# Kernel tuning notes

Hardware: AMD Instinct MI355X
Metric: run time of the kernel (lower is better)

## Reference

```python
import jax, jax.numpy as jnp
import numpy as np

B, T = 256, 20          # batch, sequence length
D = 128                 # encoder feature dim
H = 256                 # LSTM controller hidden / controller_output_size
KS = 256                # memory key/word size
MEM = 20                # memory slots
KNN = 4                 # k-NN addressing
Y = 4                   # output classes (y_dim)
EPS = 1e-8


def setup_inputs() -> dict:
    key = jax.random.key(0)
    ks = jax.random.split(key, 16)
    def kn(k, shape, fan_in):  # kaiming-normal-ish init
        return jax.random.normal(k, shape, jnp.float32) * np.float32(np.sqrt(2.0 / fan_in))
    return {
        "x": jax.random.normal(ks[0], (B, T, 32, 32), jnp.float32),
        # conv encoder
        "conv1_w": kn(ks[1], (32, 1, 4, 4), 1 * 16),  "conv1_b": jnp.zeros(32, jnp.float32),
        "conv2_w": kn(ks[2], (32, 32, 4, 4), 32 * 16), "conv2_b": jnp.zeros(32, jnp.float32),
        "conv3_w": kn(ks[3], (32, 32, 4, 4), 32 * 16), "conv3_b": jnp.zeros(32, jnp.float32),
        "fc1_w": kn(ks[4], (256, 512), 512), "fc1_b": jnp.zeros(256, jnp.float32),
        "fc2_w": kn(ks[5], (128, 256), 256), "fc2_b": jnp.zeros(128, jnp.float32),
        # context norm
        "gamma": jnp.ones(D, jnp.float32), "beta": jnp.zeros(D, jnp.float32),
        # LSTM controller: input = [z_t(128), read(256)] = 384
        "lstm_wi": kn(ks[6], (4 * H, D + KS), D + KS),
        "lstm_wh": kn(ks[7], (4 * H, H), H),
        "lstm_b": jnp.zeros(4 * H, jnp.float32),
        # head projections
        "wk": kn(ks[8], (KS, H), H),   # read key
        "wwk": kn(ks[9], (KS, H), H),  # write key
        "wv": kn(ks[10], (KS, H), H),  # write value
        # output layer on [h, read]
        "wo": kn(ks[11], (Y, H + KS), H + KS), "wo_b": jnp.zeros(Y, jnp.float32),
        "mem_init": jax.random.normal(ks[12], (MEM, KS), jnp.float32) * 0.01,
    }


def _conv(h, w, b):
    out = jax.lax.conv_general_dilated(h, w, (2, 2), [(1, 1), (1, 1)],
                                       dimension_numbers=("NCHW", "OIHW", "NCHW"))
    return jax.nn.relu(out + b[None, :, None, None])


def reference(x, conv1_w, conv1_b, conv2_w, conv2_b, conv3_w, conv3_b,
              fc1_w, fc1_b, fc2_w, fc2_b, gamma, beta,
              lstm_wi, lstm_wh, lstm_b, wk, wwk, wv, wo, wo_b, mem_init):
    b, t = x.shape[0], x.shape[1]
    # --- conv encoder on all B*T frames ---
    h = x.reshape(-1, 1, 32, 32)
    h = _conv(h, conv1_w, conv1_b)          # [BT,32,16,16]
    h = _conv(h, conv2_w, conv2_b)          # [BT,32,8,8]
    h = _conv(h, conv3_w, conv3_b)          # [BT,32,4,4]
    h = h.reshape(h.shape[0], -1)           # [BT,512] (NCHW flatten, matches torch)
    h = jax.nn.relu(h @ fc1_w.T + fc1_b)
    z = jax.nn.relu(h @ fc2_w.T + fc2_b).reshape(b, t, D)
    # --- context norm over time dim (torch var is unbiased) ---
    mu = z.mean(1)
    sigma = jnp.sqrt(z.var(1, ddof=1) + EPS)
    z = (z - mu[:, None, :]) / sigma[:, None, :] * gamma + beta
    # --- NTM-style MANN with k-NN addressing, scan over time ---
    zt = jnp.swapaxes(z, 0, 1)              # [T,B,D]
    M0 = jnp.broadcast_to(mem_init, (b, MEM, KS)) + jnp.zeros((b, MEM, KS), jnp.float32)
    carry0 = (jnp.zeros((b, H), jnp.float32), jnp.zeros((b, H), jnp.float32),
              jnp.zeros((b, KS), jnp.float32), M0)

    def step(carry, z_t):
        h_, c_, r_, M = carry
        inp = jnp.concatenate([z_t, r_], -1)
        gates = inp @ lstm_wi.T + h_ @ lstm_wh.T + lstm_b
        ig, fg, gg, og = jnp.split(gates, 4, -1)  # torch LSTM gate order i,f,g,o
        c_ = jax.nn.sigmoid(fg) * c_ + jax.nn.sigmoid(ig) * jnp.tanh(gg)
        h_ = jax.nn.sigmoid(og) * jnp.tanh(c_)
        Mn = M / (jnp.linalg.norm(M, axis=-1, keepdims=True) + EPS)
        def knn(kq):  # cosine sim -> top-k -> softmax weights
            kqn = kq / (jnp.linalg.norm(kq, axis=-1, keepdims=True) + EPS)
            sims = jnp.einsum('bd,bnd->bn', kqn, Mn)
            tv, ti = jax.lax.top_k(sims, KNN)
            return jax.nn.softmax(tv, -1), ti
        # read head
        wr, ir = knn(h_ @ wk.T)
        rows = jnp.take_along_axis(M, ir[..., None], axis=1)   # [B,KNN,KS] gather
        r_new = jnp.einsum('bk,bkd->bd', wr, rows)
        # write head: weighted scatter-add into top-k slots
        ws, iw = knn(h_ @ wwk.T)
        v = jnp.tanh(h_ @ wv.T)
        bidx = jnp.arange(M.shape[0])[:, None]
        M = M.at[bidx, iw].add(ws[..., None] * v[:, None, :])
        y = jnp.concatenate([h_, r_new], -1) @ wo.T + wo_b
        return (h_, c_, r_new, M), y

    _, ys = jax.lax.scan(step, carry0, zt)   # ys: [T,B,Y]
    y_pred_linear = ys[-1]
    return y_pred_linear, jnp.argmax(y_pred_linear, 1)
```

## Files before the change

### kernel.cpp

```cpp
#include <hip/hip_runtime.h>
#include <hip/hip_bf16.h>

#define EPSF 1e-8f

#define OFF_WIT 0
#define N_WIT   393216
#define OFF_WHT 393216
#define N_WHT   262144
#define OFF_PKT 655360
#define N_PKT   196608
#define OFF_F1T 851968
#define N_F1T   131072
#define OFF_F2T 983040
#define N_F2T   32768
#define OFF_Z   1015808
#define N_Z     655360
#define WS_FLOATS 1671168

__global__ __launch_bounds__(256) void pack_kernel(
    const float* __restrict__ wi, const float* __restrict__ wh,
    const float* __restrict__ wk, const float* __restrict__ wwk,
    const float* __restrict__ wv,
    const float* __restrict__ f1w, const float* __restrict__ f2w,
    float* __restrict__ ws) {
  int id = blockIdx.x * 256 + threadIdx.x;
  if (id < N_WIT) {
    int j = id & 3, r = (id >> 2) & 1023, k4 = id >> 12;
    ws[OFF_WIT + id] = wi[r * 384 + k4 * 4 + j];
    return;
  }
  id -= N_WIT;
  if (id < N_WHT) {
    int j = id & 3, r = (id >> 2) & 1023, k4 = id >> 12;
    ws[OFF_WHT + id] = wh[r * 256 + k4 * 4 + j];
    return;
  }
  id -= N_WHT;
  if (id < N_PKT) {
    int j = id & 3;
    int q = id >> 2;
    int c = q % 768, k4 = q / 768;
    int m = c >> 8, o = c & 255;
    int col = o * 256 + k4 * 4 + j;
    float v = (m == 0) ? wk[col] : (m == 1) ? wwk[col] : wv[col];
    ws[OFF_PKT + id] = v;
    return;
  }
  id -= N_PKT;
  if (id < N_F1T) {
    int m = id & 3, o = (id >> 2) & 255, k4 = id >> 10;
    ws[OFF_F1T + id] = f1w[o * 512 + k4 * 4 + m];
    return;
  }
  id -= N_F1T;
  if (id < N_F2T) {
    int m = id & 3, o = (id >> 2) & 127, k4 = id >> 9;
    ws[OFF_F2T + id] = f2w[o * 256 + k4 * 4 + m];
  }
}

__global__ __launch_bounds__(256) void enc_kernel(
    const float* __restrict__ x,
    const float* __restrict__ w1, const float* __restrict__ b1,
    const float* __restrict__ w2, const float* __restrict__ b2,
    const float* __restrict__ w3, const float* __restrict__ b3,
    const float* __restrict__ f1b, const float* __restrict__ f2b,
    float* __restrict__ ws) {
  __shared__ __align__(16) float xs[1024];
  __shared__ __align__(16) float c1s[512 * 19];
  __shared__ __align__(16) float c2s[256 * 9];
  __shared__ __align__(16) float c3s[512];
  __shared__ __align__(16) float h1s[256];

  const float4* __restrict__ f1T4 = (const float4*)(ws + OFF_F1T);
  const float4* __restrict__ f2T4 = (const float4*)(ws + OFF_F2T);
  float* __restrict__ z = ws + OFF_Z;

  const int f = blockIdx.x;
  const int tid = threadIdx.x;

  for (int i = tid; i < 1024; i += 256) xs[i] = x[f * 1024 + i];
  __syncthreads();

  {
    int oy = tid >> 4, ox = tid & 15;
    float patch[16];
    #pragma unroll
    for (int ky = 0; ky < 4; ++ky) {
      int iy = oy * 2 - 1 + ky;
      #pragma unroll
      for (int kx = 0; kx < 4; ++kx) {
        int ix = ox * 2 - 1 + kx;
        patch[ky * 4 + kx] =
            ((unsigned)iy <= 31u && (unsigned)ix <= 31u) ? xs[iy * 32 + ix] : 0.f;
      }
    }
    for (int oc = 0; oc < 32; ++oc) {
      float acc = b1[oc];
      #pragma unroll
      for (int k = 0; k < 16; ++k) acc = fmaf(patch[k], w1[oc * 16 + k], acc);
      c1s[(oc * 16 + oy) * 19 + ox] = fmaxf(acc, 0.f);
    }
  }
  __syncthreads();

  {
    int pix = tid & 63;
    int og = __builtin_amdgcn_readfirstlane(tid >> 6);
    int oy = pix >> 3, ox = pix & 7;
    float acc[8];
    #pragma unroll
    for (int j = 0; j < 8; ++j) acc[j] = b2[og * 8 + j];
    for (int ic = 0; ic < 32; ++ic) {
      float patch[16];
      #pragma unroll
      for (int ky = 0; ky < 4; ++ky) {
        int iy = oy * 2 - 1 + ky;
        #pragma unroll
        for (int kx = 0; kx < 4; ++kx) {
          int ix = ox * 2 - 1 + kx;
          patch[ky * 4 + kx] = ((unsigned)iy <= 15u && (unsigned)ix <= 15u)
                                   ? c1s[(ic * 16 + iy) * 19 + ix] : 0.f;
        }
      }
      #pragma unroll
      for (int j = 0; j < 8; ++j) {
        const float* wr = w2 + ((og * 8 + j) * 32 + ic) * 16;
        #pragma unroll
        for (int k = 0; k < 16; ++k) acc[j] = fmaf(patch[k], wr[k], acc[j]);
      }
    }
    #pragma unroll
    for (int j = 0; j < 8; ++j)
      c2s[((og * 8 + j) * 8 + oy) * 9 + ox] = fmaxf(acc[j], 0.f);
  }
  __syncthreads();

  {
    int pix = tid & 15, grp = tid >> 4;
    int oy = pix >> 2, ox = pix & 3;
    float a0 = b3[grp * 2], a1 = b3[grp * 2 + 1];
    for (int ic = 0; ic < 32; ++ic) {
      float patch[16];
      #pragma unroll
      for (int ky = 0; ky < 4; ++ky) {
        int iy = oy * 2 - 1 + ky;
        #pragma unroll
        for (int kx = 0; kx < 4; ++kx) {
          int ix = ox * 2 - 1 + kx;
          patch[ky * 4 + kx] = ((unsigned)iy <= 7u && (unsigned)ix <= 7u)
                                   ? c2s[(ic * 8 + iy) * 9 + ix] : 0.f;
        }
      }
      const float4* wa = (const float4*)(w3 + ((grp * 2 + 0) * 32 + ic) * 16);
      const float4* wb = (const float4*)(w3 + ((grp * 2 + 1) * 32 + ic) * 16);
      #pragma unroll
      for (int q = 0; q < 4; ++q) {
        float4 qa = wa[q], qb = wb[q];
        a0 = fmaf(patch[q * 4 + 0], qa.x, a0);
        a0 = fmaf(patch[q * 4 + 1], qa.y, a0);
        a0 = fmaf(patch[q * 4 + 2], qa.z, a0);
        a0 = fmaf(patch[q * 4 + 3], qa.w, a0);
        a1 = fmaf(patch[q * 4 + 0], qb.x, a1);
        a1 = fmaf(patch[q * 4 + 1], qb.y, a1);
        a1 = fmaf(patch[q * 4 + 2], qb.z, a1);
        a1 = fmaf(patch[q * 4 + 3], qb.w, a1);
      }
    }
    c3s[(grp * 2 + 0) * 16 + pix] = fmaxf(a0, 0.f);
    c3s[(grp * 2 + 1) * 16 + pix] = fmaxf(a1, 0.f);
  }
  __syncthreads();

  {
    float acc = f1b[tid];
    #pragma unroll 4
    for (int k4 = 0; k4 < 128; ++k4) {
      float4 cv = ((const float4*)c3s)[k4];
      float4 w = f1T4[k4 * 256 + tid];
      acc = fmaf(w.x, cv.x, acc);
      acc = fmaf(w.y, cv.y, acc);
      acc = fmaf(w.z, cv.z, acc);
      acc = fmaf(w.w, cv.w, acc);
    }
    h1s[tid] = fmaxf(acc, 0.f);
  }
  __syncthreads();

  if (tid < 128) {
    float acc = f2b[tid];
    #pragma unroll 4
    for (int k4 = 0; k4 < 64; ++k4) {
      float4 hv = ((const float4*)h1s)[k4];
      float4 w = f2T4[k4 * 128 + tid];
      acc = fmaf(w.x, hv.x, acc);
      acc = fmaf(w.y, hv.y, acc);
      acc = fmaf(w.z, hv.z, acc);
      acc = fmaf(w.w, hv.w, acc);
    }
    z[f * 128 + tid] = fmaxf(acc, 0.f);
  }
}

__global__ __launch_bounds__(256) void norm_kernel(
    float* __restrict__ ws,
    const float* __restrict__ gamma, const float* __restrict__ beta) {
  float* z = ws + OFF_Z;
  int g = blockIdx.x * 256 + threadIdx.x;
  int b = g >> 7, d = g & 127;
  float vals[20];
  float mu = 0.f;
  #pragma unroll
  for (int t = 0; t < 20; ++t) {
    float v = z[(b * 20 + t) * 128 + d];
    vals[t] = v;
    mu += v;
  }
  mu *= (1.f / 20.f);
  float var = 0.f;
  #pragma unroll
  for (int t = 0; t < 20; ++t) {
    float dd = vals[t] - mu;
    var = fmaf(dd, dd, var);
  }
  var *= (1.f / 19.f);
  float inv = 1.f / sqrtf(var + EPSF);
  float ga = gamma[d], be = beta[d];
  #pragma unroll
  for (int t = 0; t < 20; ++t)
    z[(b * 20 + t) * 128 + d] = fmaf((vals[t] - mu) * inv, ga, be);
}

__global__ __launch_bounds__(1024) void scan_kernel(
    const float* __restrict__ ws,
    const float* __restrict__ lb, const float* __restrict__ wo,
    const float* __restrict__ wob, const float* __restrict__ mem_init,
    float* __restrict__ out) {
  __shared__ float Msh[2][20 * 257];
  __shared__ __align__(16) float gsh[2][1024];
  __shared__ __align__(16) float inp[2][384];
  __shared__ __align__(16) float hsh[2][256];
  __shared__ float kqsh[2][2][256];
  __shared__ float vsh[2][256];
  __shared__ float sims[2][2][20];
  __shared__ float invq[2][2];
  __shared__ float wsel[2][2][4];
  __shared__ int isel[2][2][4];
  __shared__ float ysh[2][4];

  const int r = threadIdx.x;
  const int b0 = blockIdx.x * 2;
  const float4* wiT4 = (const float4*)(ws + OFF_WIT);
  const float4* whT4 = (const float4*)(ws + OFF_WHT);
  const float4* pkT4 = (const float4*)(ws + OFF_PKT);
  const float* zz = ws + OFF_Z;

  #pragma unroll
  for (int bl = 0; bl < 2; ++bl)
    for (int idx = r; idx < 5120; idx += 1024)
      Msh[bl][(idx >> 8) * 257 + (idx & 255)] = mem_init[idx];
  if (r < 512) {
    int bl = r >> 8, u = r & 255;
    hsh[bl][u] = 0.f;
    inp[bl][128 + u] = 0.f;
  }
  float c_reg = 0.f;
  const float bias = lb[r];
  __syncthreads();

  for (int t = 0; t < 20; ++t) {
    if (r < 256) {
      int bl = r >> 7, d = r & 127;
      inp[bl][d] = zz[((b0 + bl) * 20 + t) * 128 + d];
    }
    __syncthreads();

    float a0 = bias, a1 = bias;
    {
      const float4* ip0 = (const float4*)inp[0];
      const float4* ip1 = (const float4*)inp[1];
      #pragma unroll 8
      for (int k4 = 0; k4 < 96; ++k4) {
        float4 w = wiT4[k4 * 1024 + r];
        float4 z0 = ip0[k4], z1 = ip1[k4];
        a0 = fmaf(w.x, z0.x, a0); a1 = fmaf(w.x, z1.x, a1);
        a0 = fmaf(w.y, z0.y, a0); a1 = fmaf(w.y, z1.y, a1);
        a0 = fmaf(w.z, z0.z, a0); a1 = fmaf(w.z, z1.z, a1);
        a0 = fmaf(w.w, z0.w, a0); a1 = fmaf(w.w, z1.w, a1);
      }
      const float4* hp0 = (const float4*)hsh[0];
      const float4* hp1 = (const float4*)hsh[1];
      #pragma unroll 8
      for (int k4 = 0; k4 < 64; ++k4) {
        float4 w = whT4[k4 * 1024 + r];
        float4 h0 = hp0[k4], h1 = hp1[k4];
        a0 = fmaf(w.x, h0.x, a0); a1 = fmaf(w.x, h1.x, a1);
        a0 = fmaf(w.y, h0.y, a0); a1 = fmaf(w.y, h1.y, a1);
        a0 = fmaf(w.z, h0.z, a0); a1 = fmaf(w.z, h1.z, a1);
        a0 = fmaf(w.w, h0.w, a0); a1 = fmaf(w.w, h1.w, a1);
      }
    }
    gsh[0][r] = a0;
    gsh[1][r] = a1;
    __syncthreads();

    if (r < 512) {
      int bl = r >> 8, u = r & 255;
      float ig = gsh[bl][u], fg = gsh[bl][256 + u];
      float gg = gsh[bl][512 + u], og = gsh[bl][768 + u];
      c_reg = (1.f / (1.f + expf(-fg))) * c_reg +
              (1.f / (1.f + expf(-ig))) * tanhf(gg);
      hsh[bl][u] = (1.f / (1.f + expf(-og))) * tanhf(c_reg);
    }
    __syncthreads();

    if (r < 768) {
      int m = r >> 8, o = r & 255;
      float s0 = 0.f, s1 = 0.f;
      const float4* hp0 = (const float4*)hsh[0];
      const float4* hp1 = (const float4*)hsh[1];
      #pragma unroll 8
      for (int k4 = 0; k4 < 64; ++k4) {
        float4 w = pkT4[k4 * 768 + r];
        float4 h0 = hp0[k4], h1 = hp1[k4];
        s0 = fmaf(w.x, h0.x, s0); s1 = fmaf(w.x, h1.x, s1);
        s0 = fmaf(w.y, h0.y, s0); s1 = fmaf(w.y, h1.y, s1);
        s0 = fmaf(w.z, h0.z, s0); s1 = fmaf(w.z, h1.z, s1);
        s0 = fmaf(w.w, h0.w, s0); s1 = fmaf(w.w, h1.w, s1);
      }
      if (m < 2) {
        kqsh[0][m][o] = s0;
        kqsh[1][m][o] = s1;
      } else {
        vsh[0][o] = tanhf(s0);
        vsh[1][o] = tanhf(s1);
      }
    }
    __syncthreads();

    if (r < 320) {
      int bl = r >= 160;
      int q = bl ? r - 160 : r;
      int n = q >> 3, l = q & 7;
      const float* Mr = &Msh[bl][n * 257];
      float ss = 0.f, s1 = 0.f, s2 = 0.f;
      for (int i = 0; i < 32; ++i) {
        int k = l + 8 * i;
        float m = Mr[k];
        ss = fmaf(m, m, ss);
        s1 = fmaf(kqsh[bl][0][k], m, s1);
        s2 = fmaf(kqsh[bl][1][k], m, s2);
      }
      ss += __shfl_xor(ss, 1); s1 += __shfl_xor(s1, 1); s2 += __shfl_xor(s2, 1);
      ss += __shfl_xor(ss, 2); s1 += __shfl_xor(s1, 2); s2 += __shfl_xor(s2, 2);
      ss += __shfl_xor(ss, 4); s1 += __shfl_xor(s1, 4); s2 += __shfl_xor(s2, 4);
      if (l == 0) {
        float inv = 1.f / (sqrtf(ss) + EPSF);
        sims[bl][0][n] = s1 * inv;
        sims[bl][1][n] = s2 * inv;
      }
    } else if (r < 324) {
      int bl2 = (r - 320) >> 1, hd = r & 1;
      float qq = 0.f;
      for (int k = 0; k < 256; ++k) {
        float q = kqsh[bl2][hd][k];
        qq = fmaf(q, q, qq);
      }
      invq[bl2][hd] = 1.f / (sqrtf(qq) + EPSF);
    }
    __syncthreads();

    if (r < 4) {
      int bl = r >> 1, hd = r & 1;
      const float* sm = sims[bl][hd];
      float inv = invq[bl][hd];
      unsigned mask = 0;
      float tv[4];
      int ti[4];
      for (int j = 0; j < 4; ++j) {
        float best = -3.4e38f;
        int bx = 0;
        for (int n = 0; n < 20; ++n)
          if (!((mask >> n) & 1u) && sm[n] > best) { best = sm[n]; bx = n; }
        mask |= 1u << bx;
        tv[j] = best * inv;
        ti[j] = bx;
      }
      float e0 = 1.f;
      float e1 = expf(tv[1] - tv[0]);
      float e2 = expf(tv[2] - tv[0]);
      float e3 = expf(tv[3] - tv[0]);
      float s = e0 + e1 + e2 + e3;
      wsel[bl][hd][0] = e0 / s; wsel[bl][hd][1] = e1 / s;
      wsel[bl][hd][2] = e2 / s; wsel[bl][hd][3] = e3 / s;
      isel[bl][hd][0] = ti[0]; isel[bl][hd][1] = ti[1];
      isel[bl][hd][2] = ti[2]; isel[bl][hd][3] = ti[3];
    }
    __syncthreads();

    if (r < 512) {
      int bl = r >> 8, u = r & 255;
      float rvv = 0.f;
      #pragma unroll
      for (int j = 0; j < 4; ++j)
        rvv = fmaf(wsel[bl][0][j], Msh[bl][isel[bl][0][j] * 257 + u], rvv);
      float vv = vsh[bl][u];
      #pragma unroll
      for (int j = 0; j < 4; ++j)
        Msh[bl][isel[bl][1][j] * 257 + u] += wsel[bl][1][j] * vv;
      inp[bl][128 + u] = rvv;
    }
    __syncthreads();
  }

  if (r < 8) {
    int bl = r >> 2, o = r & 3;
    float acc = wob[o];
    const float* wr = wo + o * 512;
    for (int k = 0; k < 256; ++k) acc = fmaf(wr[k], hsh[bl][k], acc);
    for (int k = 0; k < 256; ++k) acc = fmaf(wr[256 + k], inp[bl][128 + k], acc);
    ysh[bl][o] = acc;
    out[(b0 + bl) * 4 + o] = acc;
  }
  __syncthreads();
  if (r < 2) {
    float best = ysh[r][0];
    int bx = 0;
    #pragma unroll
    for (int o = 1; o < 4; ++o)
      if (ysh[r][o] > best) { best = ysh[r][o]; bx = o; }
    out[1024 + b0 + r] = (float)bx;
  }
}

__global__ __launch_bounds__(256) void fused_kernel(
    const float* __restrict__ x,
    const float* __restrict__ w1, const float* __restrict__ b1,
    const float* __restrict__ w2, const float* __restrict__ b2,
    const float* __restrict__ w3, const float* __restrict__ b3,
    const float* __restrict__ f1w, const float* __restrict__ f1b,
    const float* __restrict__ f2w, const float* __restrict__ f2b,
    const float* __restrict__ gamma, const float* __restrict__ beta,
    const float* __restrict__ wi, const float* __restrict__ wh,
    const float* __restrict__ lb, const float* __restrict__ wk,
    const float* __restrict__ wwk, const float* __restrict__ wv,
    const float* __restrict__ wo, const float* __restrict__ wob,
    const float* __restrict__ mem_init, float* __restrict__ out) {
  __shared__ float smem[15104];
  __shared__ float simr[20], simw[20], invq[2], wsel[2][4], ysh[4];
  __shared__ int isel[2][4];
  float* z_all = smem;
  float* pool = smem + 2560;
  float* xs = pool;
  float* c1s = pool + 1024;
  float* c2s = pool + 9216;
  float* c3s = pool + 11264;
  float* h1s = pool + 11776;
  float* w1s = pool + 12032;
  float* Msh = pool;
  float* inp = pool + 5140;
  float* hsh = pool + 5524;
  float* kqr = pool + 5780;
  float* kqw = pool + 6036;
  float* vsh = pool + 6292;
  const int tid = threadIdx.x;
  const int b = blockIdx.x;
  for (int i = tid; i < 512; i += 256) w1s[i] = w1[i];
  for (int f = 0; f < 20; ++f) {
    for (int i = tid; i < 1024; i += 256) xs[i] = x[(b * 20 + f) * 1024 + i];
    __syncthreads();
    for (int i = 0; i < 32; ++i) {
      int idx = i * 256 + tid;
      int oc = idx >> 8, pix = idx & 255, oy = pix >> 4, ox = pix & 15;
      float acc = b1[oc];
      for (int ky = 0; ky < 4; ++ky) {
        int iy = oy * 2 - 1 + ky;
        if ((unsigned)iy > 31u) continue;
        for (int kx = 0; kx < 4; ++kx) {
          int ix = ox * 2 - 1 + kx;
          if ((unsigned)ix > 31u) continue;
          acc = fmaf(xs[iy * 32 + ix], w1s[oc * 16 + ky * 4 + kx], acc);
        }
      }
      c1s[idx] = fmaxf(acc, 0.f);
    }
    __syncthreads();
    {
      int oc = tid >> 3, pg = tid & 7;
      float acc[8];
      float bb = b2[oc];
      for (int i = 0; i < 8; ++i) acc[i] = bb;
      for (int ic = 0; ic < 32; ++ic) {
        const float* in = &c1s[ic * 256];
        const float* wv_ = &w2[(oc * 32 + ic) * 16];
        for (int i = 0; i < 8; ++i) {
          int p = pg + 8 * i;
          int oy = p >> 3, ox = p & 7;
          for (int ky = 0; ky < 4; ++ky) {
            int iy = oy * 2 - 1 + ky;
            if ((unsigned)iy > 15u) continue;
            for (int kx = 0; kx < 4; ++kx) {
              int ix = ox * 2 - 1 + kx;
              if ((unsigned)ix > 15u) continue;
              acc[i] = fmaf(in[iy * 16 + ix], wv_[ky * 4 + kx], acc[i]);
            }
          }
        }
      }
      for (int i = 0; i < 8; ++i) c2s[oc * 64 + pg + 8 * i] = fmaxf(acc[i], 0.f);
    }
    __syncthreads();
    {
      int oc = tid >> 3, pg = tid & 7;
      float bb = b3[oc];
      float acc0 = bb, acc1 = bb;
      int p0 = pg, p1 = pg + 8;
      int oy0 = p0 >> 2, ox0 = p0 & 3, oy1 = p1 >> 2, ox1 = p1 & 3;
      for (int ic = 0; ic < 32; ++ic) {
        const float* in = &c2s[ic * 64];
        const float* wv_ = &w3[(oc * 32 + ic) * 16];
        for (int ky = 0; ky < 4; ++ky) {
          int iy0 = oy0 * 2 - 1 + ky, iy1 = oy1 * 2 - 1 + ky;
          for (int kx = 0; kx < 4; ++kx) {
            float w = wv_[ky * 4 + kx];
            int ix0 = ox0 * 2 - 1 + kx, ix1 = ox1 * 2 - 1 + kx;
            if ((unsigned)iy0 <= 7u && (unsigned)ix0 <= 7u)
              acc0 = fmaf(in[iy0 * 8 + ix0], w, acc0);
            if ((unsigned)iy1 <= 7u && (unsigned)ix1 <= 7u)
              acc1 = fmaf(in[iy1 * 8 + ix1], w, acc1);
          }
        }
      }
      c3s[oc * 16 + p0] = fmaxf(acc0, 0.f);
      c3s[oc * 16 + p1] = fmaxf(acc1, 0.f);
    }
    __syncthreads();
    {
      float acc = f1b[tid];
      const float* wr = f1w + tid * 512;
      for (int k = 0; k < 512; ++k) acc = fmaf(wr[k], c3s[k], acc);
      h1s[tid] = fmaxf(acc, 0.f);
    }
    __syncthreads();
    if (tid < 128) {
      float acc = f2b[tid];
      const float* wr = f2w + tid * 256;
      for (int k = 0; k < 256; ++k) acc = fmaf(wr[k], h1s[k], acc);
      z_all[f * 128 + tid] = fmaxf(acc, 0.f);
    }
    __syncthreads();
  }
  if (tid < 128) {
    float mu = 0.f;
    for (int t = 0; t < 20; ++t) mu += z_all[t * 128 + tid];
    mu *= (1.f / 20.f);
    float var = 0.f;
    for (int t = 0; t < 20; ++t) {
      float dd = z_all[t * 128 + tid] - mu;
      var = fmaf(dd, dd, var);
    }
    var *= (1.f / 19.f);
    float inv = 1.f / sqrtf(var + EPSF);
    float ga = gamma[tid], be = beta[tid];
    for (int t = 0; t < 20; ++t)
      z_all[t * 128 + tid] = fmaf((z_all[t * 128 + tid] - mu) * inv, ga, be);
  }
  for (int idx = tid; idx < 20 * 256; idx += 256)
    Msh[(idx >> 8) * 257 + (idx & 255)] = mem_init[idx];
  hsh[tid] = 0.f;
  inp[128 + tid] = 0.f;
  float c_reg = 0.f;
  __syncthreads();
  const int u = tid;
  for (int t = 0; t < 20; ++t) {
    if (u < 128) inp[u] = z_all[t * 128 + u];
    __syncthreads();
    float a[4];
    for (int g = 0; g < 4; ++g) {
      int row = g * 256 + u;
      float acc = lb[row];
      const float* wr = wi + row * 384;
      for (int k = 0; k < 384; ++k) acc = fmaf(wr[k], inp[k], acc);
      const float* hr = wh + row * 256;
      for (int k = 0; k < 256; ++k) acc = fmaf(hr[k], hsh[k], acc);
      a[g] = acc;
    }
    __syncthreads();
    {
      float ig = 1.f / (1.f + expf(-a[0]));
      float fg = 1.f / (1.f + expf(-a[1]));
      float gg = tanhf(a[2]);
      float og = 1.f / (1.f + expf(-a[3]));
      c_reg = fg * c_reg + ig * gg;
      hsh[u] = og * tanhf(c_reg);
    }
    __syncthreads();
    {
      float sk = 0.f, sw = 0.f, sv = 0.f;
      const float* rk = wk + u * 256;
      const float* rw = wwk + u * 256;
      const float* rv = wv + u * 256;
      for (int k = 0; k < 256; ++k) {
        float hv = hsh[k];
        sk = fmaf(rk[k], hv, sk);
        sw = fmaf(rw[k], hv, sw);
        sv = fmaf(rv[k], hv, sv);
      }
      kqr[u] = sk;
      kqw[u] = sw;
      vsh[u] = tanhf(sv);
    }
    __syncthreads();
    if (u < 20) {
      const float* Mr = &Msh[u * 257];
      float ss = 0.f, s1 = 0.f, s2 = 0.f;
      for (int k = 0; k < 256; ++k) {
        float m = Mr[k];
        ss = fmaf(m, m, ss);
        s1 = fmaf(kqr[k], m, s1);
        s2 = fmaf(kqw[k], m, s2);
      }
      float inv = 1.f / (sqrtf(ss) + EPSF);
      simr[u] = s1 * inv;
      simw[u] = s2 * inv;
    } else if (u == 20 || u == 21) {
      const float* q = (u == 20) ? kqr : kqw;
      float qq = 0.f;
      for (int k = 0; k < 256; ++k) qq = fmaf(q[k], q[k], qq);
      invq[u - 20] = 1.f / (sqrtf(qq) + EPSF);
    }
    __syncthreads();
    if (u < 2) {
      const float* sims = (u == 0) ? simr : simw;
      float inv = invq[u];
      unsigned mask = 0;
      float tv[4];
      int ti[4];
      for (int j = 0; j < 4; ++j) {
        float best = -3.4e38f;
        int bx = 0;
        for (int n = 0; n < 20; ++n)
          if (!((mask >> n) & 1u) && sims[n] > best) { best = sims[n]; bx = n; }
        mask |= 1u << bx;
        tv[j] = best * inv;
        ti[j] = bx;
      }
      float e1 = expf(tv[1] - tv[0]);
      float e2 = expf(tv[2] - tv[0]);
      float e3 = expf(tv[3] - tv[0]);
      float s = 1.f + e1 + e2 + e3;
      wsel[u][0] = 1.f / s; wsel[u][1] = e1 / s; wsel[u][2] = e2 / s; wsel[u][3] = e3 / s;
      isel[u][0] = ti[0]; isel[u][1] = ti[1]; isel[u][2] = ti[2]; isel[u][3] = ti[3];
    }
    __syncthreads();
    {
      float rvv = 0.f;
      for (int j = 0; j < 4; ++j)
        rvv = fmaf(wsel[0][j], Msh[isel[0][j] * 257 + u], rvv);
      float vv = vsh[u];
      for (int j = 0; j < 4; ++j)
        Msh[isel[1][j] * 257 + u] += wsel[1][j] * vv;
      inp[128 + u] = rvv;
    }
    __syncthreads();
  }
  if (u < 4) {
    float acc = wob[u];
    const float* wr = wo + u * 512;
    for (int k = 0; k < 256; ++k) acc = fmaf(wr[k], hsh[k], acc);
    for (int k = 0; k < 256; ++k) acc = fmaf(wr[256 + k], inp[128 + k], acc);
    ysh[u] = acc;
    out[b * 4 + u] = acc;
  }
  __syncthreads();
  if (u == 0) {
    float best = ysh[0];
    int bx = 0;
    for (int o = 1; o < 4; ++o)
      if (ysh[o] > best) { best = ysh[o]; bx = o; }
    out[1024 + b] = (float)bx;
  }
}

extern "C" void kernel_launch(void* const* d_in, const int* in_sizes, int n_in,
                              void* d_out, int out_size, void* d_ws, size_t ws_size,
                              hipStream_t stream) {
  const float* x    = (const float*)d_in[0];
  const float* c1w  = (const float*)d_in[1];
  const float* c1b  = (const float*)d_in[2];
  const float* c2w  = (const float*)d_in[3];
  const float* c2b  = (const float*)d_in[4];
  const float* c3w  = (const float*)d_in[5];
  const float* c3b  = (const float*)d_in[6];
  const float* f1w  = (const float*)d_in[7];
  const float* f1b  = (const float*)d_in[8];
  const float* f2w  = (const float*)d_in[9];
  const float* f2b  = (const float*)d_in[10];
  const float* gam  = (const float*)d_in[11];
  const float* bet  = (const float*)d_in[12];
  const float* wi   = (const float*)d_in[13];
  const float* wh   = (const float*)d_in[14];
  const float* lb   = (const float*)d_in[15];
  const float* wk   = (const float*)d_in[16];
  const float* wwk  = (const float*)d_in[17];
  const float* wv   = (const float*)d_in[18];
  const float* wo   = (const float*)d_in[19];
  const float* wob  = (const float*)d_in[20];
  const float* mem0 = (const float*)d_in[21];
  float* out = (float*)d_out;

  if (ws_size >= (size_t)WS_FLOATS * sizeof(float)) {
    float* ws = (float*)d_ws;
    pack_kernel<<<3968, 256, 0, stream>>>(wi, wh, wk, wwk, wv, f1w, f2w, ws);
    enc_kernel<<<5120, 256, 0, stream>>>(x, c1w, c1b, c2w, c2b, c3w, c3b,
                                         f1b, f2b, ws);
    norm_kernel<<<128, 256, 0, stream>>>(ws, gam, bet);
    scan_kernel<<<128, 1024, 0, stream>>>(ws, lb, wo, wob, mem0, out);
  } else {
    fused_kernel<<<256, 256, 0, stream>>>(x, c1w, c1b, c2w, c2b, c3w, c3b,
                                          f1w, f1b, f2w, f2b, gam, bet,
                                          wi, wh, lb, wk, wwk, wv, wo, wob,
                                          mem0, out);
  }
}
```

Before: 1.336 ms.

## Precompute input-to-gate projection of encoder features outside the recurrent scan

Adds a gz_kernel that computes the z_t part of the LSTM input projection (plus bias) for all batch-time frames at once. It uses register tiling over 16 frames so each weight load is reused across them. The scan kernel then starts each step from these precomputed gate values and only runs the read-vector and hidden-state parts of the matvec inside the sequential loop. This takes a third of the input-weight streaming off the critical recurrent path, at the cost of a 20MB workspace buffer and an extra launch. It also raises the unroll factor on the encoder FC loops and adds a min-blocks hint to the scan kernel's launch bounds.

```diff
diff --git a/kernel.cpp b/kernel.cpp
--- a/kernel.cpp
+++ b/kernel.cpp
@@ -15,7 +15,10 @@
 #define N_F2T   32768
 #define OFF_Z   1015808
 #define N_Z     655360
-#define WS_FLOATS 1671168
+#define WS_BASE 1671168
+#define OFF_GZ  1671168
+#define N_GZ    5242880
+#define WS_FULL 6914048
 
 __global__ __launch_bounds__(256) void pack_kernel(
     const float* __restrict__ wi, const float* __restrict__ wh,
@@ -174,7 +177,7 @@
 
   {
     float acc = f1b[tid];
-    #pragma unroll 4
+    #pragma unroll 8
     for (int k4 = 0; k4 < 128; ++k4) {
       float4 cv = ((const float4*)c3s)[k4];
       float4 w = f1T4[k4 * 256 + tid];
@@ -189,7 +192,7 @@
 
   if (tid < 128) {
     float acc = f2b[tid];
-    #pragma unroll 4
+    #pragma unroll 8
     for (int k4 = 0; k4 < 64; ++k4) {
       float4 hv = ((const float4*)h1s)[k4];
       float4 w = f2T4[k4 * 128 + tid];
@@ -231,8 +234,48 @@
     z[(b * 20 + t) * 128 + d] = fmaf((vals[t] - mu) * inv, ga, be);
 }
 
-__global__ __launch_bounds__(1024) void scan_kernel(
-    const float* __restrict__ ws,
+__global__ __launch_bounds__(512) void gz_kernel(
+    const float* __restrict__ ws, const float* __restrict__ lb,
+    float* __restrict__ gz) {
+  __shared__ __align__(16) float zs[16][128];
+  const float4* wiT4 = (const float4*)(ws + OFF_WIT);
+  const float* zz = ws + OFF_Z;
+  const int tid = threadIdx.x;
+  const int f0 = blockIdx.x * 16;
+
+  for (int i = tid; i < 2048; i += 512) zs[i >> 7][i & 127] = zz[f0 * 128 + i];
+  __syncthreads();
+
+  float acc0[16], acc1[16];
+  const float b0v = lb[tid], b1v = lb[tid + 512];
+  #pragma unroll
+  for (int f = 0; f < 16; ++f) { acc0[f] = b0v; acc1[f] = b1v; }
+
+  for (int k4 = 0; k4 < 32; ++k4) {
+    float4 w0 = wiT4[k4 * 1024 + tid];
+    float4 w1 = wiT4[k4 * 1024 + tid + 512];
+    #pragma unroll
+    for (int f = 0; f < 16; ++f) {
+      float4 zv = *(const float4*)&zs[f][k4 * 4];
+      acc0[f] = fmaf(w0.x, zv.x, acc0[f]);
+      acc0[f] = fmaf(w0.y, zv.y, acc0[f]);
+      acc0[f] = fmaf(w0.z, zv.z, acc0[f]);
+      acc0[f] = fmaf(w0.w, zv.w, acc0[f]);
+      acc1[f] = fmaf(w1.x, zv.x, acc1[f]);
+      acc1[f] = fmaf(w1.y, zv.y, acc1[f]);
+      acc1[f] = fmaf(w1.z, zv.z, acc1[f]);
+      acc1[f] = fmaf(w1.w, zv.w, acc1[f]);
+    }
+  }
+  #pragma unroll
+  for (int f = 0; f < 16; ++f) {
+    gz[(f0 + f) * 1024 + tid] = acc0[f];
+    gz[(f0 + f) * 1024 + 512 + tid] = acc1[f];
+  }
+}
+
+__global__ __launch_bounds__(1024, 2) void scan_kernel(
+    const float* __restrict__ ws, const float* __restrict__ gz,
     const float* __restrict__ lb, const float* __restrict__ wo,
     const float* __restrict__ wob, const float* __restrict__ mem_init,
     float* __restrict__ out) {
@@ -254,6 +297,7 @@
   const float4* whT4 = (const float4*)(ws + OFF_WHT);
   const float4* pkT4 = (const float4*)(ws + OFF_PKT);
   const float* zz = ws + OFF_Z;
+  const int k4s = gz ? 32 : 0;
 
   #pragma unroll
   for (int bl = 0; bl < 2; ++bl)
@@ -269,18 +313,25 @@
   __syncthreads();
 
   for (int t = 0; t < 20; ++t) {
-    if (r < 256) {
+    if (!gz && r < 256) {
       int bl = r >> 7, d = r & 127;
       inp[bl][d] = zz[((b0 + bl) * 20 + t) * 128 + d];
     }
     __syncthreads();
 
-    float a0 = bias, a1 = bias;
+    float a0, a1;
+    if (gz) {
+      a0 = gz[(b0 * 20 + t) * 1024 + r];
+      a1 = gz[((b0 + 1) * 20 + t) * 1024 + r];
+    } else {
+      a0 = bias;
+      a1 = bias;
+    }
     {
       const float4* ip0 = (const float4*)inp[0];
       const float4* ip1 = (const float4*)inp[1];
       #pragma unroll 8
-      for (int k4 = 0; k4 < 96; ++k4) {
+      for (int k4 = k4s; k4 < 96; ++k4) {
         float4 w = wiT4[k4 * 1024 + r];
         float4 z0 = ip0[k4], z1 = ip1[k4];
         a0 = fmaf(w.x, z0.x, a0); a1 = fmaf(w.x, z1.x, a1);
@@ -709,13 +760,19 @@
   const float* mem0 = (const float*)d_in[21];
   float* out = (float*)d_out;
 
-  if (ws_size >= (size_t)WS_FLOATS * sizeof(float)) {
+  if (ws_size >= (size_t)WS_BASE * sizeof(float)) {
     float* ws = (float*)d_ws;
+    const bool full = ws_size >= (size_t)WS_FULL * sizeof(float);
     pack_kernel<<<3968, 256, 0, stream>>>(wi, wh, wk, wwk, wv, f1w, f2w, ws);
     enc_kernel<<<5120, 256, 0, stream>>>(x, c1w, c1b, c2w, c2b, c3w, c3b,
                                          f1b, f2b, ws);
     norm_kernel<<<128, 256, 0, stream>>>(ws, gam, bet);
-    scan_kernel<<<128, 1024, 0, stream>>>(ws, lb, wo, wob, mem0, out);
+    const float* gz = nullptr;
+    if (full) {
+      gz_kernel<<<320, 512, 0, stream>>>(ws, lb, ws + OFF_GZ);
+      gz = ws + OFF_GZ;
+    }
+    scan_kernel<<<128, 1024, 0, stream>>>(ws, gz, lb, wo, wob, mem0, out);
   } else {
     fused_kernel<<<256, 256, 0, stream>>>(x, c1w, c1b, c2w, c2b, c3w, c3b,
                                           f1w, f1b, f2w, f2b, gam, bet,
```

Result: no change. 1.312 ms (-1.8%).
